# Performance work log

Measured on AMD Instinct MI355X. Metric: run time of the kernel, lower is better.

## Reference

```python
import jax, jax.numpy as jnp
import numpy as np

N_NODES = 50000
N_EDGES = 800000
D_FEAT = 256
HIDDEN = 256
N_CLASSES = 10
N_GRAPHS = 128


def setup_inputs() -> dict:
    key = jax.random.key(0)
    ks = jax.random.split(key, 16)
    x = jax.random.normal(ks[0], (N_NODES, D_FEAT), dtype=jnp.float32)
    edge_index = jax.random.randint(ks[1], (2, N_EDGES), 0, N_NODES, dtype=jnp.int64)
    batch = jnp.sort(jax.random.randint(ks[2], (N_NODES,), 0, N_GRAPHS, dtype=jnp.int64))
    def lin(k, fin, fout):
        s = 1.0 / np.sqrt(fin)
        return jax.random.uniform(k, (fin, fout), jnp.float32, -s, s)
    return {
        "x": x, "edge_index": edge_index, "batch": batch,
        "W0": lin(ks[3], D_FEAT, HIDDEN), "b0": jnp.zeros((HIDDEN,), jnp.float32),
        "W1": lin(ks[4], HIDDEN, HIDDEN), "b1": jnp.zeros((HIDDEN,), jnp.float32),
        "W2": lin(ks[5], HIDDEN, HIDDEN), "b2": jnp.zeros((HIDDEN,), jnp.float32),
        "fc1_W": lin(ks[6], HIDDEN, HIDDEN), "fc1_b": jnp.zeros((HIDDEN,), jnp.float32),
        "fc2_W": lin(ks[7], HIDDEN, N_CLASSES), "fc2_b": jnp.zeros((N_CLASSES,), jnp.float32),
    }


def _gcn_norm(edge_index, n_nodes):
    # PyG GCNConv: add self-loops, deg from (A+I) with unit weights,
    # norm_e = deg^{-1/2}[src] * deg^{-1/2}[dst]
    loop = jnp.arange(n_nodes, dtype=edge_index.dtype)
    src = jnp.concatenate([edge_index[0], loop])
    dst = jnp.concatenate([edge_index[1], loop])
    deg = jax.ops.segment_sum(jnp.ones_like(dst, dtype=jnp.float32), dst,
                              num_segments=n_nodes)
    dinv = jnp.where(deg > 0, jax.lax.rsqrt(deg), 0.0)
    norm = dinv[src] * dinv[dst]
    return src, dst, norm


def _gcn_conv(x, src, dst, norm, W, b, n_nodes):
    h = x @ W                              # [N, out]
    msg = h[src] * norm[:, None]           # gather + scale  [E+N, out]
    out = jax.ops.segment_sum(msg, dst, num_segments=n_nodes)  # scatter-add
    return out + b


def reference(x, edge_index, batch, W0, b0, W1, b1, W2, b2, fc1_W, fc1_b, fc2_W, fc2_b):
    n_nodes = x.shape[0]
    src, dst, norm = _gcn_norm(edge_index, n_nodes)
    h = jax.nn.relu(_gcn_conv(x, src, dst, norm, W0, b0, n_nodes))
    h = jax.nn.relu(_gcn_conv(h, src, dst, norm, W1, b1, n_nodes))
    h = jax.nn.relu(_gcn_conv(h, src, dst, norm, W2, b2, n_nodes))
    # global add pool over graphs
    g = jax.ops.segment_sum(h, batch, num_segments=N_GRAPHS)   # [G, H]
    g = jax.nn.relu(g @ fc1_W + fc1_b)
    # dropout p=0.5 is identity in eval mode
    logits = g @ fc2_W + fc2_b
    return jax.nn.log_softmax(logits, axis=-1)
```

## Files before the change

### kernel.cpp

```cpp
#include <hip/hip_runtime.h>
#include <math.h>

#define FDIM 256
#define NGRAPH 128
#define NCLASS 10

typedef short short8 __attribute__((ext_vector_type(8)));
typedef float floatx4 __attribute__((ext_vector_type(4)));

static __device__ __forceinline__ unsigned short f2bf(float f) {
    unsigned u = __float_as_uint(f);
    u += 0x7FFF + ((u >> 16) & 1);
    return (unsigned short)(u >> 16);
}


__global__ __launch_bounds__(256) void prep_kernel(const int* __restrict__ dst,
                                                   int* __restrict__ cnt,
                                                   unsigned short* __restrict__ slot,
                                                   int E, int nCnt,
                                                   const float* __restrict__ W0,
                                                   const float* __restrict__ W1,
                                                   const float* __restrict__ W2,
                                                   unsigned short* __restrict__ Bp0,
                                                   unsigned short* __restrict__ Bp1,
                                                   unsigned short* __restrict__ Bp2,
                                                   float4* __restrict__ g4) {
    const int b = blockIdx.x;
    const int t = threadIdx.x;
    if (b < nCnt) {
        int e = b * 256 + t;
        if (e < E) slot[e] = (unsigned short)atomicAdd(&cnt[dst[e]], 1);
        return;
    }
    const int b2 = b - nCnt;
    if (b2 >= 96) {
        g4[(size_t)(b2 - 96) * 256 + t] = (float4){0.f, 0.f, 0.f, 0.f};
        return;
    }
    const float* W = (b2 < 32) ? W0 : (b2 < 64) ? W1 : W2;
    unsigned short* Bp = (b2 < 32) ? Bp0 : (b2 < 64) ? Bp1 : Bp2;
    int idx = (b2 & 31) * 256 + t;
    int kstep = idx >> 10;
    int ntile = (idx >> 6) & 15;
    int lane  = idx & 63;
    int col   = ntile * 16 + (lane & 15);
    int krow  = kstep * 32 + (lane >> 4) * 8;
    unsigned short o[8];
#pragma unroll
    for (int j = 0; j < 8; j++) o[j] = f2bf(W[(size_t)(krow + j) * FDIM + col]);
    *(uint4*)(Bp + (size_t)idx * 8) = *(uint4*)o;
}


__global__ __launch_bounds__(256) void csr_bsum(const int* __restrict__ cnt,
                                                int* __restrict__ bsum, int N) {
    __shared__ int red[256];
    const int t = threadIdx.x;
    const int base = blockIdx.x * 1024 + t * 4;
    int s = 0;
#pragma unroll
    for (int i = 0; i < 4; i++)
        if (base + i < N) s += cnt[base + i];
    red[t] = s;
    __syncthreads();
    for (int off = 128; off > 0; off >>= 1) {
        if (t < off) red[t] += red[t + off];
        __syncthreads();
    }
    if (t == 0) bsum[blockIdx.x] = red[0];
}

__global__ __launch_bounds__(256) void csr_scan2(const int* __restrict__ cnt,
                                                 const int* __restrict__ bsum,
                                                 int* __restrict__ rowptr,
                                                 float* __restrict__ dinv, int N, int E) {
    __shared__ int redo[256];
    __shared__ int tsum[256];
    const int t = threadIdx.x;
    const int bid = blockIdx.x;

    int pre = 0;
    for (int i = t; i < bid; i += 256) pre += bsum[i];
    redo[t] = pre;
    __syncthreads();
    for (int off = 128; off > 0; off >>= 1) {
        if (t < off) redo[t] += redo[t + off];
        __syncthreads();
    }
    const int blockoff = redo[0];
    __syncthreads();

    const int base = bid * 1024 + t * 4;
    int c[4];
    int s = 0;
#pragma unroll
    for (int i = 0; i < 4; i++) {
        c[i] = (base + i < N) ? cnt[base + i] : 0;
        s += c[i];
    }
    tsum[t] = s;
    __syncthreads();
    for (int off = 1; off < 256; off <<= 1) {
        int v = (t >= off) ? tsum[t - off] : 0;
        __syncthreads();
        tsum[t] += v;
        __syncthreads();
    }
    int run = blockoff + ((t == 0) ? 0 : tsum[t - 1]);
#pragma unroll
    for (int i = 0; i < 4; i++) {
        int idx = base + i;
        if (idx < N) {
            rowptr[idx] = run;
            dinv[idx] = rsqrtf((float)c[i] + 1.0f);
            run += c[i];
        }
    }
    if (bid == 0 && t == 0) rowptr[N] = E;
}


template<int AFP32>
static __device__ __forceinline__ void gemm_tile64(const void* __restrict__ A,
                                                   const unsigned short* __restrict__ Bp,
                                                   unsigned short* __restrict__ C,
                                                   int M, int tile) {
    const int wave = threadIdx.x >> 6;
    const int lane = threadIdx.x & 63;
    const int quad = lane >> 4;
    const int m    = lane & 15;
    const int row0 = tile * 64;

    short8 breg[8][4];
#pragma unroll
    for (int ks = 0; ks < 8; ks++)
#pragma unroll
        for (int j = 0; j < 4; j++)
            breg[ks][j] = *(const short8*)((const short*)Bp +
                            ((size_t)((ks * 16 + wave * 4 + j) * 64 + lane) * 8));

#pragma unroll
    for (int mt = 0; mt < 4; mt++) {
        const int r0 = min(row0 + mt * 16 + m, M - 1);
        floatx4 acc[4];
#pragma unroll
        for (int j = 0; j < 4; j++) acc[j] = (floatx4){0.f, 0.f, 0.f, 0.f};
#pragma unroll
        for (int ks = 0; ks < 8; ks++) {
            short8 a;
            if (AFP32) {
                const float* ar = (const float*)A + (size_t)r0 * FDIM + ks * 32 + quad * 8;
                float4 p0 = *(const float4*)ar;
                float4 p1 = *(const float4*)(ar + 4);
                a[0] = (short)f2bf(p0.x); a[1] = (short)f2bf(p0.y);
                a[2] = (short)f2bf(p0.z); a[3] = (short)f2bf(p0.w);
                a[4] = (short)f2bf(p1.x); a[5] = (short)f2bf(p1.y);
                a[6] = (short)f2bf(p1.z); a[7] = (short)f2bf(p1.w);
            } else {
                a = *(const short8*)((const short*)A + (size_t)r0 * FDIM + ks * 32 + quad * 8);
            }
#pragma unroll
            for (int j = 0; j < 4; j++)
                acc[j] = __builtin_amdgcn_mfma_f32_16x16x32_bf16(a, breg[ks][j], acc[j], 0, 0, 0);
        }
#pragma unroll
        for (int j = 0; j < 4; j++) {
            int col = (wave * 4 + j) * 16 + m;
#pragma unroll
            for (int r = 0; r < 4; r++) {
                int row = row0 + mt * 16 + quad * 4 + r;
                if (row < M) C[(size_t)row * FDIM + col] = f2bf(acc[j][r]);
            }
        }
    }
}

__global__ __launch_bounds__(256, 2) void gemm0_fill_kernel(const float* __restrict__ x,
                                                            const unsigned short* __restrict__ Bp0,
                                                            unsigned short* __restrict__ H,
                                                            int M, int ng,
                                                            const int* __restrict__ src,
                                                            const int* __restrict__ dst,
                                                            const int* __restrict__ rowptr,
                                                            const unsigned short* __restrict__ slot,
                                                            unsigned short* __restrict__ srcs, int E) {
    if ((int)blockIdx.x < ng) {
        gemm_tile64<1>(x, Bp0, H, M, blockIdx.x);
        return;
    }
    int e = (blockIdx.x - ng) * 256 + threadIdx.x;
    if (e < E) srcs[rowptr[dst[e]] + (int)slot[e]] = (unsigned short)src[e];
}

__global__ __launch_bounds__(256, 2) void mfma_gemm(const unsigned short* __restrict__ A,
                                                    const unsigned short* __restrict__ Bp,
                                                    unsigned short* __restrict__ C, int M) {
    gemm_tile64<0>(A, Bp, C, M, blockIdx.x);
}


static __device__ __forceinline__ void accum8(float* acc, uint4 v, float nm) {
    const unsigned* u = (const unsigned*)&v;
#pragma unroll
    for (int i = 0; i < 4; i++) {
        acc[2 * i]     += nm * __uint_as_float(u[i] << 16);
        acc[2 * i + 1] += nm * __uint_as_float(u[i] & 0xFFFF0000u);
    }
}

static __device__ __forceinline__ void gather_node(const unsigned short* __restrict__ h,
                                                   const int* __restrict__ rowptr,
                                                   const unsigned short* __restrict__ srcs,
                                                   const float* __restrict__ dinv,
                                                   const float* __restrict__ bias,
                                                   int node, int lane, float* acc) {
    const float di = dinv[node];
    {
        uint4 sv = *(const uint4*)(h + (size_t)node * FDIM + lane * 8);
        const unsigned* u = (const unsigned*)&sv;
#pragma unroll
        for (int i = 0; i < 4; i++) {
            acc[2 * i]     = di * di * __uint_as_float(u[i] << 16);
            acc[2 * i + 1] = di * di * __uint_as_float(u[i] & 0xFFFF0000u);
        }
        float4 b0 = *(const float4*)(bias + lane * 8);
        float4 b1 = *(const float4*)(bias + lane * 8 + 4);
        acc[0] += b0.x; acc[1] += b0.y; acc[2] += b0.z; acc[3] += b0.w;
        acc[4] += b1.x; acc[5] += b1.y; acc[6] += b1.z; acc[7] += b1.w;
    }
    const int beg = rowptr[node];
    const int end = rowptr[node + 1];
    int p = beg;
    for (; p + 4 <= end; p += 4) {
        int s0 = srcs[p], s1 = srcs[p + 1], s2 = srcs[p + 2], s3 = srcs[p + 3];
        float n0 = dinv[s0] * di, n1 = dinv[s1] * di;
        float n2 = dinv[s2] * di, n3 = dinv[s3] * di;
        uint4 v0 = *(const uint4*)(h + (size_t)s0 * FDIM + lane * 8);
        uint4 v1 = *(const uint4*)(h + (size_t)s1 * FDIM + lane * 8);
        uint4 v2 = *(const uint4*)(h + (size_t)s2 * FDIM + lane * 8);
        uint4 v3 = *(const uint4*)(h + (size_t)s3 * FDIM + lane * 8);
        accum8(acc, v0, n0);
        accum8(acc, v1, n1);
        accum8(acc, v2, n2);
        accum8(acc, v3, n3);
    }
    for (; p < end; p++) {
        int s = srcs[p];
        float nm = dinv[s] * di;
        uint4 v = *(const uint4*)(h + (size_t)s * FDIM + lane * 8);
        accum8(acc, v, nm);
    }
#pragma unroll
    for (int i = 0; i < 8; i++) acc[i] = fmaxf(acc[i], 0.0f);
}

__global__ __launch_bounds__(256) void gather_kernel(const unsigned short* __restrict__ h,
                                                     const int* __restrict__ rowptr,
                                                     const unsigned short* __restrict__ srcs,
                                                     const float* __restrict__ dinv,
                                                     const float* __restrict__ bias,
                                                     unsigned short* __restrict__ out, int N) {
    const int node = blockIdx.x * 8 + (threadIdx.x >> 5);
    const int lane = threadIdx.x & 31;
    if (node >= N) return;
    float acc[8];
    gather_node(h, rowptr, srcs, dinv, bias, node, lane, acc);
    unsigned short o[8];
#pragma unroll
    for (int i = 0; i < 8; i++) o[i] = f2bf(acc[i]);
    *(uint4*)(out + (size_t)node * FDIM + lane * 8) = *(uint4*)o;
}

__global__ __launch_bounds__(256) void gather_pool_kernel(const unsigned short* __restrict__ h,
                                                          const int* __restrict__ rowptr,
                                                          const unsigned short* __restrict__ srcs,
                                                          const float* __restrict__ dinv,
                                                          const float* __restrict__ bias,
                                                          const int* __restrict__ batch,
                                                          float* __restrict__ g, int N) {
    __shared__ float red[8][FDIM];
    __shared__ int bid[8];
    const int hw   = threadIdx.x >> 5;
    const int lane = threadIdx.x & 31;
    const int node = blockIdx.x * 8 + hw;

    float acc[8] = {0.f, 0.f, 0.f, 0.f, 0.f, 0.f, 0.f, 0.f};
    if (node < N) gather_node(h, rowptr, srcs, dinv, bias, node, lane, acc);
#pragma unroll
    for (int i = 0; i < 8; i++) red[hw][lane * 8 + i] = acc[i];
    if (lane == 0) bid[hw] = (node < N) ? batch[node] : -1;
    __syncthreads();

    const int f = threadIdx.x;
    int cur = -1;
    float run = 0.0f;
    for (int i = 0; i < 8; i++) {
        int b = bid[i];
        if (b < 0) break;
        if (b != cur) {
            if (cur >= 0) atomicAdd(&g[(size_t)cur * FDIM + f], run);
            cur = b;
            run = 0.0f;
        }
        run += red[i][f];
    }
    if (cur >= 0) atomicAdd(&g[(size_t)cur * FDIM + f], run);
}


__global__ __launch_bounds__(256) void fc_head_kernel(const float* __restrict__ g,
                                                      const float* __restrict__ fc1W,
                                                      const float* __restrict__ fc1b,
                                                      const float* __restrict__ fc2W,
                                                      const float* __restrict__ fc2b,
                                                      float* __restrict__ out) {
    __shared__ float gs[FDIM];
    __shared__ float part[4][FDIM];
    __shared__ float hs[FDIM];
    __shared__ float p2[256];
    __shared__ float logits[NCLASS];
    const int r = blockIdx.x;
    const int t = threadIdx.x;
    const int w = t >> 6;
    const int l = t & 63;

    gs[t] = g[(size_t)r * FDIM + t];
    __syncthreads();

    float a[4] = {0.f, 0.f, 0.f, 0.f};
    for (int kk = 0; kk < 64; kk++) {
        int k = w * 64 + kk;
        float gv = gs[k];
#pragma unroll
        for (int j = 0; j < 4; j++) a[j] += gv * fc1W[(size_t)k * FDIM + j * 64 + l];
    }
#pragma unroll
    for (int j = 0; j < 4; j++) part[w][j * 64 + l] = a[j];
    __syncthreads();

    float s1 = part[0][t] + part[1][t] + part[2][t] + part[3][t] + fc1b[t];
    hs[t] = fmaxf(s1, 0.0f);
    __syncthreads();

    float a2 = 0.0f;
    const int c = t & 15;
    if (c < NCLASS) {
        int k0 = (t >> 4) * 16;
        for (int kk = 0; kk < 16; kk++)
            a2 += hs[k0 + kk] * fc2W[(size_t)(k0 + kk) * NCLASS + c];
    }
    p2[t] = a2;
    __syncthreads();

    if (t < NCLASS) {
        float s2 = fc2b[t];
        for (int seg = 0; seg < 16; seg++) s2 += p2[seg * 16 + t];
        logits[t] = s2;
    }
    __syncthreads();

    if (t == 0) {
        float mx = logits[0];
        for (int cc = 1; cc < NCLASS; cc++) mx = fmaxf(mx, logits[cc]);
        float ssum = 0.0f;
        for (int cc = 0; cc < NCLASS; cc++) ssum += expf(logits[cc] - mx);
        float lse = mx + logf(ssum);
        for (int cc = 0; cc < NCLASS; cc++) out[(size_t)r * NCLASS + cc] = logits[cc] - lse;
    }
}


extern "C" void kernel_launch(void* const* d_in, const int* in_sizes, int n_in,
                              void* d_out, int out_size, void* d_ws, size_t ws_size,
                              hipStream_t stream) {
    const float* x     = (const float*)d_in[0];
    const int*   ei    = (const int*)d_in[1];
    const int*   batch = (const int*)d_in[2];
    const float* W0 = (const float*)d_in[3];  const float* b0 = (const float*)d_in[4];
    const float* W1 = (const float*)d_in[5];  const float* b1 = (const float*)d_in[6];
    const float* W2 = (const float*)d_in[7];  const float* b2 = (const float*)d_in[8];
    const float* fc1W = (const float*)d_in[9];  const float* fc1b = (const float*)d_in[10];
    const float* fc2W = (const float*)d_in[11]; const float* fc2b = (const float*)d_in[12];
    float* out = (float*)d_out;

    const int N = in_sizes[0] / FDIM;
    const int E = in_sizes[1] / 2;
    const int* src = ei;
    const int* dst = ei + E;
    const int Mpad = ((N + 63) / 64) * 64;
    const int nb   = (N + 1023) / 1024;
    const int nCnt = (E + 255) / 256;
    const int ng   = (N + 63) / 64;

    char* p = (char*)d_ws;
    unsigned short* S  = (unsigned short*)p; p += (size_t)Mpad * FDIM * 2;
    unsigned short* H  = (unsigned short*)p; p += (size_t)Mpad * FDIM * 2;
    unsigned short* Wp0 = (unsigned short*)p; p += (size_t)8192 * 8 * 2;
    unsigned short* Wp1 = (unsigned short*)p; p += (size_t)8192 * 8 * 2;
    unsigned short* Wp2 = (unsigned short*)p; p += (size_t)8192 * 8 * 2;
    float* dinv = (float*)p; p += (size_t)N * 4;
    int*   cnt  = (int*)p;   p += (size_t)N * 4;
    int*   rowptr = (int*)p; p += (size_t)(N + 4) * 4;
    int*   bsum = (int*)p;   p += (size_t)256 * 4;
    unsigned short* srcs = (unsigned short*)p; p += (((size_t)E * 2 + 15) & ~15ull);
    unsigned short* slot = (unsigned short*)p; p += (((size_t)E * 2 + 15) & ~15ull);
    float* g    = (float*)p;

    hipMemsetAsync(cnt, 0, (size_t)N * sizeof(int), stream);
    prep_kernel<<<nCnt + 128, 256, 0, stream>>>(dst, cnt, slot, E, nCnt,
                                                W0, W1, W2, Wp0, Wp1, Wp2, (float4*)g);
    csr_bsum<<<nb, 256, 0, stream>>>(cnt, bsum, N);
    csr_scan2<<<nb, 256, 0, stream>>>(cnt, bsum, rowptr, dinv, N, E);

    gemm0_fill_kernel<<<ng + nCnt, 256, 0, stream>>>(x, Wp0, H, N, ng,
                                                     src, dst, rowptr, slot, srcs, E);

    gather_kernel<<<(N + 7) / 8, 256, 0, stream>>>(H, rowptr, srcs, dinv, b0, S, N);
    mfma_gemm<<<ng, 256, 0, stream>>>(S, Wp1, H, N);
    gather_kernel<<<(N + 7) / 8, 256, 0, stream>>>(H, rowptr, srcs, dinv, b1, S, N);
    mfma_gemm<<<ng, 256, 0, stream>>>(S, Wp2, H, N);
    gather_pool_kernel<<<(N + 7) / 8, 256, 0, stream>>>(H, rowptr, srcs, dinv, b2,
                                                        batch, g, N);
    fc_head_kernel<<<NGRAPH, 256, 0, stream>>>(g, fc1W, fc1b, fc2W, fc2b, out);
}
```

Before: 421.9 us.

## Pad CSR rows to 8, precompute edge norms, use full-wave gather per node

CSR row lengths are padded to multiples of 8 so the gather can read 8 source indices and 8 precomputed edge norms with vector loads and issue 8 independent row loads per iteration, with no remainder loop. Each edge's norm is computed once in the fill kernel instead of on every layer. The gather now uses a full 64-lane wave per node with 4 features per lane and a wave-uniform node index. In exchange it adds two memsets over the padded arrays and up to 7 wasted zero-weight loads of row 0 per node.

```diff
diff --git a/kernel.cpp b/kernel.cpp
--- a/kernel.cpp
+++ b/kernel.cpp
@@ -13,6 +13,8 @@
     u += 0x7FFF + ((u >> 16) & 1);
     return (unsigned short)(u >> 16);
 }
+static __device__ __forceinline__ float bflo(unsigned u) { return __uint_as_float(u << 16); }
+static __device__ __forceinline__ float bfhi(unsigned u) { return __uint_as_float(u & 0xFFFF0000u); }
 
 
 __global__ __launch_bounds__(256) void prep_kernel(const int* __restrict__ dst,
@@ -61,7 +63,7 @@
     int s = 0;
 #pragma unroll
     for (int i = 0; i < 4; i++)
-        if (base + i < N) s += cnt[base + i];
+        if (base + i < N) s += (cnt[base + i] + 7) & ~7;
     red[t] = s;
     __syncthreads();
     for (int off = 128; off > 0; off >>= 1) {
@@ -74,7 +76,7 @@
 __global__ __launch_bounds__(256) void csr_scan2(const int* __restrict__ cnt,
                                                  const int* __restrict__ bsum,
                                                  int* __restrict__ rowptr,
-                                                 float* __restrict__ dinv, int N, int E) {
+                                                 float* __restrict__ dinv, int N) {
     __shared__ int redo[256];
     __shared__ int tsum[256];
     const int t = threadIdx.x;
@@ -92,12 +94,13 @@
     __syncthreads();
 
     const int base = bid * 1024 + t * 4;
-    int c[4];
+    int c[4], pc[4];
     int s = 0;
 #pragma unroll
     for (int i = 0; i < 4; i++) {
         c[i] = (base + i < N) ? cnt[base + i] : 0;
-        s += c[i];
+        pc[i] = (c[i] + 7) & ~7;
+        s += pc[i];
     }
     tsum[t] = s;
     __syncthreads();
@@ -114,10 +117,10 @@
         if (idx < N) {
             rowptr[idx] = run;
             dinv[idx] = rsqrtf((float)c[i] + 1.0f);
-            run += c[i];
+            run += pc[i];
+            if (idx == N - 1) rowptr[N] = run;
         }
     }
-    if (bid == 0 && t == 0) rowptr[N] = E;
 }
 
 
@@ -184,13 +187,20 @@
                                                             const int* __restrict__ dst,
                                                             const int* __restrict__ rowptr,
                                                             const unsigned short* __restrict__ slot,
-                                                            unsigned short* __restrict__ srcs, int E) {
+                                                            unsigned short* __restrict__ srcs,
+                                                            float* __restrict__ normv,
+                                                            const float* __restrict__ dinv, int E) {
     if ((int)blockIdx.x < ng) {
         gemm_tile64<1>(x, Bp0, H, M, blockIdx.x);
         return;
     }
     int e = (blockIdx.x - ng) * 256 + threadIdx.x;
-    if (e < E) srcs[rowptr[dst[e]] + (int)slot[e]] = (unsigned short)src[e];
+    if (e < E) {
+        int s = src[e], d = dst[e];
+        int r = rowptr[d] + (int)slot[e];
+        srcs[r] = (unsigned short)s;
+        normv[r] = dinv[s] * dinv[d];
+    }
 }
 
 __global__ __launch_bounds__(256, 2) void mfma_gemm(const unsigned short* __restrict__ A,
@@ -200,102 +210,91 @@
 }
 
 
-static __device__ __forceinline__ void accum8(float* acc, uint4 v, float nm) {
-    const unsigned* u = (const unsigned*)&v;
-#pragma unroll
-    for (int i = 0; i < 4; i++) {
-        acc[2 * i]     += nm * __uint_as_float(u[i] << 16);
-        acc[2 * i + 1] += nm * __uint_as_float(u[i] & 0xFFFF0000u);
-    }
-}
-
-static __device__ __forceinline__ void gather_node(const unsigned short* __restrict__ h,
-                                                   const int* __restrict__ rowptr,
-                                                   const unsigned short* __restrict__ srcs,
-                                                   const float* __restrict__ dinv,
-                                                   const float* __restrict__ bias,
-                                                   int node, int lane, float* acc) {
+static __device__ __forceinline__ void gather_node64(const unsigned short* __restrict__ h,
+                                                     const int* __restrict__ rowptr,
+                                                     const unsigned short* __restrict__ srcs,
+                                                     const float* __restrict__ normv,
+                                                     const float* __restrict__ dinv,
+                                                     const float* __restrict__ bias,
+                                                     int node, int lane, float* acc) {
     const float di = dinv[node];
-    {
-        uint4 sv = *(const uint4*)(h + (size_t)node * FDIM + lane * 8);
-        const unsigned* u = (const unsigned*)&sv;
-#pragma unroll
-        for (int i = 0; i < 4; i++) {
-            acc[2 * i]     = di * di * __uint_as_float(u[i] << 16);
-            acc[2 * i + 1] = di * di * __uint_as_float(u[i] & 0xFFFF0000u);
-        }
-        float4 b0 = *(const float4*)(bias + lane * 8);
-        float4 b1 = *(const float4*)(bias + lane * 8 + 4);
-        acc[0] += b0.x; acc[1] += b0.y; acc[2] += b0.z; acc[3] += b0.w;
-        acc[4] += b1.x; acc[5] += b1.y; acc[6] += b1.z; acc[7] += b1.w;
-    }
+    const float dii = di * di;
+    uint2 sv = *(const uint2*)(h + (size_t)node * FDIM + lane * 4);
+    float4 b = *(const float4*)(bias + lane * 4);
+    acc[0] = dii * bflo(sv.x) + b.x;
+    acc[1] = dii * bfhi(sv.x) + b.y;
+    acc[2] = dii * bflo(sv.y) + b.z;
+    acc[3] = dii * bfhi(sv.y) + b.w;
+
     const int beg = rowptr[node];
     const int end = rowptr[node + 1];
-    int p = beg;
-    for (; p + 4 <= end; p += 4) {
-        int s0 = srcs[p], s1 = srcs[p + 1], s2 = srcs[p + 2], s3 = srcs[p + 3];
-        float n0 = dinv[s0] * di, n1 = dinv[s1] * di;
-        float n2 = dinv[s2] * di, n3 = dinv[s3] * di;
-        uint4 v0 = *(const uint4*)(h + (size_t)s0 * FDIM + lane * 8);
-        uint4 v1 = *(const uint4*)(h + (size_t)s1 * FDIM + lane * 8);
-        uint4 v2 = *(const uint4*)(h + (size_t)s2 * FDIM + lane * 8);
-        uint4 v3 = *(const uint4*)(h + (size_t)s3 * FDIM + lane * 8);
-        accum8(acc, v0, n0);
-        accum8(acc, v1, n1);
-        accum8(acc, v2, n2);
-        accum8(acc, v3, n3);
-    }
-    for (; p < end; p++) {
-        int s = srcs[p];
-        float nm = dinv[s] * di;
-        uint4 v = *(const uint4*)(h + (size_t)s * FDIM + lane * 8);
-        accum8(acc, v, nm);
-    }
-#pragma unroll
-    for (int i = 0; i < 8; i++) acc[i] = fmaxf(acc[i], 0.0f);
+    for (int p = beg; p < end; p += 8) {
+        uint4 s8 = *(const uint4*)(srcs + p);
+        float4 n0 = *(const float4*)(normv + p);
+        float4 n1 = *(const float4*)(normv + p + 4);
+        const unsigned short* sp = (const unsigned short*)&s8;
+        uint2 v[8];
+#pragma unroll
+        for (int i = 0; i < 8; i++)
+            v[i] = *(const uint2*)(h + (size_t)sp[i] * FDIM + lane * 4);
+        float nm[8] = {n0.x, n0.y, n0.z, n0.w, n1.x, n1.y, n1.z, n1.w};
+#pragma unroll
+        for (int i = 0; i < 8; i++) {
+            acc[0] += nm[i] * bflo(v[i].x);
+            acc[1] += nm[i] * bfhi(v[i].x);
+            acc[2] += nm[i] * bflo(v[i].y);
+            acc[3] += nm[i] * bfhi(v[i].y);
+        }
+    }
+#pragma unroll
+    for (int i = 0; i < 4; i++) acc[i] = fmaxf(acc[i], 0.0f);
 }
 
 __global__ __launch_bounds__(256) void gather_kernel(const unsigned short* __restrict__ h,
                                                      const int* __restrict__ rowptr,
                                                      const unsigned short* __restrict__ srcs,
+                                                     const float* __restrict__ normv,
                                                      const float* __restrict__ dinv,
                                                      const float* __restrict__ bias,
                                                      unsigned short* __restrict__ out, int N) {
-    const int node = blockIdx.x * 8 + (threadIdx.x >> 5);
-    const int lane = threadIdx.x & 31;
+    int node = blockIdx.x * 4 + (threadIdx.x >> 6);
+    node = __builtin_amdgcn_readfirstlane(node);
+    const int lane = threadIdx.x & 63;
     if (node >= N) return;
-    float acc[8];
-    gather_node(h, rowptr, srcs, dinv, bias, node, lane, acc);
-    unsigned short o[8];
-#pragma unroll
-    for (int i = 0; i < 8; i++) o[i] = f2bf(acc[i]);
-    *(uint4*)(out + (size_t)node * FDIM + lane * 8) = *(uint4*)o;
+    float acc[4];
+    gather_node64(h, rowptr, srcs, normv, dinv, bias, node, lane, acc);
+    unsigned short o[4];
+#pragma unroll
+    for (int i = 0; i < 4; i++) o[i] = f2bf(acc[i]);
+    *(uint2*)(out + (size_t)node * FDIM + lane * 4) = *(uint2*)o;
 }
 
 __global__ __launch_bounds__(256) void gather_pool_kernel(const unsigned short* __restrict__ h,
                                                           const int* __restrict__ rowptr,
                                                           const unsigned short* __restrict__ srcs,
+                                                          const float* __restrict__ normv,
                                                           const float* __restrict__ dinv,
                                                           const float* __restrict__ bias,
                                                           const int* __restrict__ batch,
                                                           float* __restrict__ g, int N) {
-    __shared__ float red[8][FDIM];
-    __shared__ int bid[8];
-    const int hw   = threadIdx.x >> 5;
-    const int lane = threadIdx.x & 31;
-    const int node = blockIdx.x * 8 + hw;
-
-    float acc[8] = {0.f, 0.f, 0.f, 0.f, 0.f, 0.f, 0.f, 0.f};
-    if (node < N) gather_node(h, rowptr, srcs, dinv, bias, node, lane, acc);
-#pragma unroll
-    for (int i = 0; i < 8; i++) red[hw][lane * 8 + i] = acc[i];
+    __shared__ float red[4][FDIM];
+    __shared__ int bid[4];
+    const int hw   = threadIdx.x >> 6;
+    const int lane = threadIdx.x & 63;
+    int node = blockIdx.x * 4 + hw;
+    node = __builtin_amdgcn_readfirstlane(node);
+
+    float acc[4] = {0.f, 0.f, 0.f, 0.f};
+    if (node < N) gather_node64(h, rowptr, srcs, normv, dinv, bias, node, lane, acc);
+#pragma unroll
+    for (int i = 0; i < 4; i++) red[hw][lane * 4 + i] = acc[i];
     if (lane == 0) bid[hw] = (node < N) ? batch[node] : -1;
     __syncthreads();
 
     const int f = threadIdx.x;
     int cur = -1;
     float run = 0.0f;
-    for (int i = 0; i < 8; i++) {
+    for (int i = 0; i < 4; i++) {
         int b = bid[i];
         if (b < 0) break;
         if (b != cur) {
@@ -392,6 +391,7 @@
     const int nb   = (N + 1023) / 1024;
     const int nCnt = (E + 255) / 256;
     const int ng   = (N + 63) / 64;
+    const size_t Epad = (size_t)E + 8 * (size_t)N;
 
     char* p = (char*)d_ws;
     unsigned short* S  = (unsigned short*)p; p += (size_t)Mpad * FDIM * 2;
@@ -403,24 +403,27 @@
     int*   cnt  = (int*)p;   p += (size_t)N * 4;
     int*   rowptr = (int*)p; p += (size_t)(N + 4) * 4;
     int*   bsum = (int*)p;   p += (size_t)256 * 4;
-    unsigned short* srcs = (unsigned short*)p; p += (((size_t)E * 2 + 15) & ~15ull);
+    unsigned short* srcs = (unsigned short*)p; p += ((Epad * 2 + 15) & ~15ull);
     unsigned short* slot = (unsigned short*)p; p += (((size_t)E * 2 + 15) & ~15ull);
+    float* normv = (float*)p; p += ((Epad * 4 + 15) & ~15ull);
     float* g    = (float*)p;
 
     hipMemsetAsync(cnt, 0, (size_t)N * sizeof(int), stream);
+    hipMemsetAsync(srcs, 0, Epad * 2, stream);
+    hipMemsetAsync(normv, 0, Epad * 4, stream);
     prep_kernel<<<nCnt + 128, 256, 0, stream>>>(dst, cnt, slot, E, nCnt,
                                                 W0, W1, W2, Wp0, Wp1, Wp2, (float4*)g);
     csr_bsum<<<nb, 256, 0, stream>>>(cnt, bsum, N);
-    csr_scan2<<<nb, 256, 0, stream>>>(cnt, bsum, rowptr, dinv, N, E);
+    csr_scan2<<<nb, 256, 0, stream>>>(cnt, bsum, rowptr, dinv, N);
 
     gemm0_fill_kernel<<<ng + nCnt, 256, 0, stream>>>(x, Wp0, H, N, ng,
-                                                     src, dst, rowptr, slot, srcs, E);
-
-    gather_kernel<<<(N + 7) / 8, 256, 0, stream>>>(H, rowptr, srcs, dinv, b0, S, N);
+                                                     src, dst, rowptr, slot, srcs, normv, dinv, E);
+
+    gather_kernel<<<(N + 3) / 4, 256, 0, stream>>>(H, rowptr, srcs, normv, dinv, b0, S, N);
     mfma_gemm<<<ng, 256, 0, stream>>>(S, Wp1, H, N);
-    gather_kernel<<<(N + 7) / 8, 256, 0, stream>>>(H, rowptr, srcs, dinv, b1, S, N);
+    gather_kernel<<<(N + 3) / 4, 256, 0, stream>>>(H, rowptr, srcs, normv, dinv, b1, S, N);
     mfma_gemm<<<ng, 256, 0, stream>>>(S, Wp2, H, N);
-    gather_pool_kernel<<<(N + 7) / 8, 256, 0, stream>>>(H, rowptr, srcs, dinv, b2,
+    gather_pool_kernel<<<(N + 3) / 4, 256, 0, stream>>>(H, rowptr, srcs, normv, dinv, b2,
                                                         batch, g, N);
     fc_head_kernel<<<NGRAPH, 256, 0, stream>>>(g, fc1W, fc1b, fc2W, fc2b, out);
 }
```

Measured after the change: 436.8 us. +3.5%, slower.
